# Performance work log

Measured on AMD Instinct MI355X. Metric: run time of the kernel, lower is better.

Reference implementation:

```python
import jax, jax.numpy as jnp
import numpy as np

NEG_SLOPE = 0.2

def gat_conv(x, W, att_src, att_dst, src, dst, num_nodes, concat):
    # x: [N, F_in], W: [F_in, H*C], att_*: [H, C]
    H, C = att_src.shape
    h = (x @ W).reshape(-1, H, C)                      # [N, H, C]
    a_src = jnp.sum(h * att_src[None], axis=-1)        # [N, H]
    a_dst = jnp.sum(h * att_dst[None], axis=-1)        # [N, H]
    # per-edge raw attention: alpha_j (source) + alpha_i (target)
    alpha = a_src[src] + a_dst[dst]                    # [E, H]
    alpha = jax.nn.leaky_relu(alpha, NEG_SLOPE)
    # segment softmax over incoming edges of each destination node
    amax = jax.ops.segment_max(alpha, dst, num_segments=num_nodes)  # [N, H]
    amax = jnp.where(jnp.isfinite(amax), amax, 0.0)
    ex = jnp.exp(alpha - amax[dst])                    # [E, H]
    denom = jax.ops.segment_sum(ex, dst, num_segments=num_nodes)    # [N, H]
    attn = ex / (denom[dst] + 1e-16)                   # [E, H]
    # attention-weighted scatter-add aggregation
    msg = h[src] * attn[..., None]                     # [E, H, C]
    out = jax.ops.segment_sum(msg, dst, num_segments=num_nodes)     # [N, H, C]
    if concat:
        return out.reshape(num_nodes, H * C)
    return out.mean(axis=1)


def setup_inputs() -> dict:
    key = jax.random.key(0)
    ks = jax.random.split(key, 8)
    N, E = 100000, 1600000
    F_in, Hid, Hd, F_out = 256, 32, 8, 64
    glorot = lambda k, shape: jax.random.uniform(
        k, shape, jnp.float32, -1.0, 1.0) * jnp.sqrt(6.0 / (shape[0] + shape[-1]))
    x = jax.random.normal(ks[0], (N, F_in), jnp.float32)
    edge_index = jax.random.randint(ks[1], (2, E), 0, N, jnp.int64)
    W1 = glorot(ks[2], (F_in, Hd * Hid))
    att_src1 = glorot(ks[3], (Hd, Hid))
    att_dst1 = glorot(ks[4], (Hd, Hid))
    W2 = glorot(ks[5], (Hd * Hid, 1 * F_out))
    att_src2 = glorot(ks[6], (1, F_out))
    att_dst2 = glorot(ks[7], (1, F_out))
    return {"x": x, "W1": W1, "att_src1": att_src1, "att_dst1": att_dst1,
            "W2": W2, "att_src2": att_src2, "att_dst2": att_dst2,
            "edge_index": edge_index}


def reference(x, W1, att_src1, att_dst1, W2, att_src2, att_dst2, edge_index):
    src, dst = edge_index[0], edge_index[1]
    N = x.shape[0]
    # dropout is inactive in eval mode
    h = gat_conv(x, W1, att_src1, att_dst1, src, dst, N, concat=True)
    h = jax.nn.elu(h)
    out = gat_conv(h, W2, att_src2, att_dst2, src, dst, N, concat=False)
    return out
```

## Files before the change

kernel.cpp:

```cpp
#include <hip/hip_runtime.h>
#include <hip/hip_bf16.h>

#define LRELU(a) ((a) >= 0.0f ? (a) : 0.2f * (a))

typedef __attribute__((ext_vector_type(8))) _Float16 f16x8;
typedef __attribute__((ext_vector_type(4))) _Float16 f16x4;
typedef __attribute__((ext_vector_type(4))) float f32x4;

__global__ __launch_bounds__(256) void cvt_w_t(const float* __restrict__ W,
                                               _Float16* __restrict__ T,
                                               int K, int Nc) {
    int t = blockIdx.x * 256 + threadIdx.x;
    if (t >= K * Nc) return;
    int k = t / Nc, n = t % Nc;
    T[n * K + k] = (_Float16)W[t];
}

__global__ __launch_bounds__(512) void gemm1_mfma(
    const float* __restrict__ A,
    const _Float16* __restrict__ BT,
    const float* __restrict__ attS, const float* __restrict__ attD,
    _Float16* __restrict__ C, float* __restrict__ a_src, float* __restrict__ a_dst,
    int M) {
    const int K = 256;
    __shared__ _Float16 sA[128][40];
    __shared__ _Float16 sB[256][40];
    int tid = threadIdx.x;
    int m0 = blockIdx.y * 128;
    int wid = tid >> 6, lane = tid & 63;
    int wm = (wid >> 2) * 64, wn = (wid & 3) * 64;
    int lr = lane & 15, lg = lane >> 4;

    f32x4 acc[4][4];
    #pragma unroll
    for (int i = 0; i < 4; ++i)
        #pragma unroll
        for (int j = 0; j < 4; ++j)
            acc[i][j] = (f32x4){0.f, 0.f, 0.f, 0.f};

    for (int k0 = 0; k0 < K; k0 += 32) {
        {
            int row = tid >> 2, seg = tid & 3;
            int grow = m0 + row;
            float4 v0 = make_float4(0.f, 0.f, 0.f, 0.f), v1 = v0;
            if (grow < M) {
                v0 = *(const float4*)&A[(size_t)grow * K + k0 + seg * 8];
                v1 = *(const float4*)&A[(size_t)grow * K + k0 + seg * 8 + 4];
            }
            f16x8 hv;
            hv[0] = (_Float16)v0.x; hv[1] = (_Float16)v0.y;
            hv[2] = (_Float16)v0.z; hv[3] = (_Float16)v0.w;
            hv[4] = (_Float16)v1.x; hv[5] = (_Float16)v1.y;
            hv[6] = (_Float16)v1.z; hv[7] = (_Float16)v1.w;
            *(f16x8*)&sA[row][seg * 8] = hv;
        }
        #pragma unroll
        for (int rnd = 0; rnd < 2; ++rnd) {
            int idx = tid + rnd * 512;
            int row = idx >> 2, seg = idx & 3;
            *(f16x8*)&sB[row][seg * 8] = *(const f16x8*)&BT[(size_t)row * K + k0 + seg * 8];
        }
        __syncthreads();
        f16x8 bfr[4];
        #pragma unroll
        for (int i = 0; i < 4; ++i)
            bfr[i] = *(const f16x8*)&sB[wn + i * 16 + lr][lg * 8];
        #pragma unroll
        for (int mi = 0; mi < 4; ++mi) {
            f16x8 av = *(const f16x8*)&sA[wm + mi * 16 + lr][lg * 8];
            #pragma unroll
            for (int ni = 0; ni < 4; ++ni)
                acc[mi][ni] = __builtin_amdgcn_mfma_f32_16x16x32_f16(av, bfr[ni], acc[mi][ni], 0, 0, 0);
        }
        __syncthreads();
    }

    float asv[4], adv[4];
    #pragma unroll
    for (int ni = 0; ni < 4; ++ni) {
        int col = wn + ni * 16 + lr;
        asv[ni] = attS[col];
        adv[ni] = attD[col];
    }
    int head0 = wn >> 5;
    #pragma unroll
    for (int mi = 0; mi < 4; ++mi) {
        #pragma unroll
        for (int r = 0; r < 4; ++r) {
            int row = m0 + wm + mi * 16 + lg * 4 + r;
            float v0 = acc[mi][0][r], v1 = acc[mi][1][r];
            float v2 = acc[mi][2][r], v3 = acc[mi][3][r];
            float ps0 = v0 * asv[0] + v1 * asv[1], pd0 = v0 * adv[0] + v1 * adv[1];
            float ps1 = v2 * asv[2] + v3 * asv[3], pd1 = v2 * adv[2] + v3 * adv[3];
            #pragma unroll
            for (int msk = 8; msk >= 1; msk >>= 1) {
                ps0 += __shfl_xor(ps0, msk); pd0 += __shfl_xor(pd0, msk);
                ps1 += __shfl_xor(ps1, msk); pd1 += __shfl_xor(pd1, msk);
            }
            if (row < M) {
                C[(size_t)row * 256 + wn +  0 + lr] = (_Float16)v0;
                C[(size_t)row * 256 + wn + 16 + lr] = (_Float16)v1;
                C[(size_t)row * 256 + wn + 32 + lr] = (_Float16)v2;
                C[(size_t)row * 256 + wn + 48 + lr] = (_Float16)v3;
                if (lr == 0) {
                    a_src[(size_t)row * 8 + head0]     = ps0;
                    a_dst[(size_t)row * 8 + head0]     = pd0;
                    a_src[(size_t)row * 8 + head0 + 1] = ps1;
                    a_dst[(size_t)row * 8 + head0 + 1] = pd1;
                }
            }
        }
    }
}

__global__ __launch_bounds__(256) void gemm2_mfma(
    const _Float16* __restrict__ A,
    const _Float16* __restrict__ BT,
    const float* __restrict__ attS, const float* __restrict__ attD,
    _Float16* __restrict__ C, float* __restrict__ a_src, float* __restrict__ a_dst,
    int M) {
    const int K = 256;
    __shared__ _Float16 sA[128][40];
    __shared__ _Float16 sB[64][40];
    int tid = threadIdx.x;
    int m0 = blockIdx.y * 128;
    int wid = tid >> 6, lane = tid & 63;
    int wm = wid * 32;
    int lr = lane & 15, lg = lane >> 4;

    f32x4 acc[2][4];
    #pragma unroll
    for (int i = 0; i < 2; ++i)
        #pragma unroll
        for (int j = 0; j < 4; ++j)
            acc[i][j] = (f32x4){0.f, 0.f, 0.f, 0.f};

    for (int k0 = 0; k0 < K; k0 += 32) {
        #pragma unroll
        for (int rnd = 0; rnd < 2; ++rnd) {
            int idx = tid + rnd * 256;
            int row = idx >> 2, seg = idx & 3;
            int grow = m0 + row;
            f16x8 va = {0, 0, 0, 0, 0, 0, 0, 0};
            if (grow < M) va = *(const f16x8*)&A[(size_t)grow * K + k0 + seg * 8];
            *(f16x8*)&sA[row][seg * 8] = va;
        }
        {
            int row = tid >> 2, seg = tid & 3;
            *(f16x8*)&sB[row][seg * 8] = *(const f16x8*)&BT[(size_t)row * K + k0 + seg * 8];
        }
        __syncthreads();
        f16x8 bfr[4];
        #pragma unroll
        for (int i = 0; i < 4; ++i)
            bfr[i] = *(const f16x8*)&sB[i * 16 + lr][lg * 8];
        #pragma unroll
        for (int mi = 0; mi < 2; ++mi) {
            f16x8 av = *(const f16x8*)&sA[wm + mi * 16 + lr][lg * 8];
            #pragma unroll
            for (int ni = 0; ni < 4; ++ni)
                acc[mi][ni] = __builtin_amdgcn_mfma_f32_16x16x32_f16(av, bfr[ni], acc[mi][ni], 0, 0, 0);
        }
        __syncthreads();
    }

    float asv[4], adv[4];
    #pragma unroll
    for (int ni = 0; ni < 4; ++ni) {
        asv[ni] = attS[ni * 16 + lr];
        adv[ni] = attD[ni * 16 + lr];
    }
    #pragma unroll
    for (int mi = 0; mi < 2; ++mi) {
        #pragma unroll
        for (int r = 0; r < 4; ++r) {
            int row = m0 + wm + mi * 16 + lg * 4 + r;
            float ps = 0.f, pd = 0.f;
            #pragma unroll
            for (int ni = 0; ni < 4; ++ni) {
                float v = acc[mi][ni][r];
                ps += v * asv[ni];
                pd += v * adv[ni];
            }
            #pragma unroll
            for (int msk = 8; msk >= 1; msk >>= 1) {
                ps += __shfl_xor(ps, msk);
                pd += __shfl_xor(pd, msk);
            }
            if (row < M) {
                #pragma unroll
                for (int ni = 0; ni < 4; ++ni)
                    C[(size_t)row * 64 + ni * 16 + lr] = (_Float16)acc[mi][ni][r];
                if (lr == 0) { a_src[row] = ps; a_dst[row] = pd; }
            }
        }
    }
}

__global__ __launch_bounds__(256) void hist_dst(const int* __restrict__ dst, unsigned* __restrict__ cnt, int E) {
    int e = blockIdx.x * 256 + threadIdx.x;
    if (e < E) atomicAdd(&cnt[dst[e]], 1u);
}

__global__ __launch_bounds__(256) void scan_partial(const unsigned* __restrict__ cnt,
                                                    int* __restrict__ rowptr,
                                                    unsigned* __restrict__ bsum, int n) {
    __shared__ unsigned s[256];
    int i = blockIdx.x * 256 + threadIdx.x;
    unsigned v = (i < n) ? cnt[i] : 0u;
    s[threadIdx.x] = v;
    __syncthreads();
    #pragma unroll
    for (int off = 1; off < 256; off <<= 1) {
        unsigned t = (threadIdx.x >= off) ? s[threadIdx.x - off] : 0u;
        __syncthreads();
        s[threadIdx.x] += t;
        __syncthreads();
    }
    if (i < n) rowptr[i + 1] = (int)s[threadIdx.x];
    if (threadIdx.x == 255) bsum[blockIdx.x] = s[255];
}

__global__ __launch_bounds__(512) void scan_bsum(unsigned* __restrict__ bsum, int nb) {
    __shared__ unsigned s[512];
    int t = threadIdx.x;
    s[t] = (t < nb) ? bsum[t] : 0u;
    __syncthreads();
    #pragma unroll
    for (int off = 1; off < 512; off <<= 1) {
        unsigned v = (t >= off) ? s[t - off] : 0u;
        __syncthreads();
        s[t] += v;
        __syncthreads();
    }
    unsigned ex = (t == 0) ? 0u : s[t - 1];
    if (t < nb) bsum[t] = ex;
}

__global__ __launch_bounds__(256) void scan_add(int* __restrict__ rowptr, const unsigned* __restrict__ boff, int n) {
    int i = blockIdx.x * 256 + threadIdx.x;
    if (i < n) rowptr[i + 1] += (int)boff[blockIdx.x];
    if (blockIdx.x == 0 && threadIdx.x == 0) rowptr[0] = 0;
}

__global__ __launch_bounds__(256) void scatter_srcs(const int* __restrict__ src, const int* __restrict__ dst,
                                                    const int* __restrict__ rowptr,
                                                    unsigned* __restrict__ cnt, int* __restrict__ srcs, int E) {
    int e = blockIdx.x * 256 + threadIdx.x;
    if (e >= E) return;
    int d = dst[e];
    unsigned p = atomicAdd(&cnt[d], 1u);
    srcs[rowptr[d] + (int)p] = src[e];
}

__global__ __launch_bounds__(256) void agg1(const int* __restrict__ srcs,
                                            const int* __restrict__ rowptr,
                                            const float* __restrict__ a_src,
                                            const float* __restrict__ a_dst,
                                            const _Float16* __restrict__ h1,
                                            _Float16* __restrict__ o1, int N) {
    int wid = threadIdx.x >> 6;
    int lane = threadIdx.x & 63;
    int d = blockIdx.x * 4 + wid;
    if (d >= N) return;
    int beg = rowptr[d], end = rowptr[d + 1];
    int e8 = lane & 7;
    int hd = lane >> 3;
    float adst = a_dst[(size_t)d * 8 + hd];
    const char* h1b = (const char*)h1;
    const char* asb = (const char*)a_src;
    unsigned loff = (unsigned)(lane << 3);

    float4 acc = make_float4(0.f, 0.f, 0.f, 0.f);
    float wsum = 0.0f;
    for (int j0 = beg; j0 < end; j0 += 8) {
        int nb = end - j0; if (nb > 8) nb = 8;
        int s2 = 0; float w = 0.f;
        if (e8 < nb) {
            s2 = srcs[j0 + e8];
            float a = *(const float*)(asb + (((unsigned)s2 << 5) + ((unsigned)hd << 2))) + adst;
            a = LRELU(a);
            w = __expf(a);
        }
        wsum += w;
        #pragma unroll 8
        for (int t = 0; t < 8; ++t) {
            if (t >= nb) break;
            int sl = (lane & 56) | t;
            float at = __shfl(w, sl);
            int s = __shfl(s2, sl);
            f16x4 hq = *(const f16x4*)(h1b + (((unsigned)s << 9) + loff));
            acc.x += (float)hq[0] * at;
            acc.y += (float)hq[1] * at;
            acc.z += (float)hq[2] * at;
            acc.w += (float)hq[3] * at;
        }
    }
    wsum += __shfl_xor(wsum, 1);
    wsum += __shfl_xor(wsum, 2);
    wsum += __shfl_xor(wsum, 4);
    float rw = 1.0f / (wsum + 1e-16f);
    acc.x *= rw; acc.y *= rw; acc.z *= rw; acc.w *= rw;
    acc.x = acc.x > 0.0f ? acc.x : expm1f(acc.x);
    acc.y = acc.y > 0.0f ? acc.y : expm1f(acc.y);
    acc.z = acc.z > 0.0f ? acc.z : expm1f(acc.z);
    acc.w = acc.w > 0.0f ? acc.w : expm1f(acc.w);
    f16x4 hh;
    hh[0] = (_Float16)acc.x;
    hh[1] = (_Float16)acc.y;
    hh[2] = (_Float16)acc.z;
    hh[3] = (_Float16)acc.w;
    *(f16x4*)(o1 + (size_t)d * 256 + lane * 4) = hh;
}

__global__ __launch_bounds__(256) void agg2(const int* __restrict__ srcs,
                                            const int* __restrict__ rowptr,
                                            const float* __restrict__ a_src,
                                            const float* __restrict__ a_dst,
                                            const _Float16* __restrict__ h2,
                                            float* __restrict__ out, int N) {
    int wid = threadIdx.x >> 6;
    int lane = threadIdx.x & 63;
    int d = blockIdx.x * 4 + wid;
    if (d >= N) return;
    int beg = rowptr[d], end = rowptr[d + 1];
    float adst = a_dst[d];
    const char* h2b = (const char*)h2;
    int grp = lane >> 4;
    int cid = lane & 15;

    float4 acc = make_float4(0.f, 0.f, 0.f, 0.f);
    float wsum = 0.0f;
    for (int j0 = beg; j0 < end; j0 += 64) {
        int nb = end - j0; if (nb > 64) nb = 64;
        int s2 = 0; float w = 0.f;
        if (lane < nb) {
            s2 = srcs[j0 + lane];
            float a = LRELU(a_src[s2] + adst);
            w = __expf(a);
        }
        wsum += w;
        int tmax = (nb + 3) >> 2;
        for (int t = 0; t < tmax; ++t) {
            int ei = 4 * t + grp;
            float at = __shfl(w, ei);
            int s = __shfl(s2, ei);
            f16x4 hv = *(const f16x4*)(h2b + (((unsigned)s << 7) + ((unsigned)cid << 3)));
            acc.x += (float)hv[0] * at;
            acc.y += (float)hv[1] * at;
            acc.z += (float)hv[2] * at;
            acc.w += (float)hv[3] * at;
        }
    }
    #pragma unroll
    for (int mask = 16; mask <= 32; mask <<= 1) {
        acc.x += __shfl_xor(acc.x, mask);
        acc.y += __shfl_xor(acc.y, mask);
        acc.z += __shfl_xor(acc.z, mask);
        acc.w += __shfl_xor(acc.w, mask);
    }
    #pragma unroll
    for (int mask = 1; mask < 64; mask <<= 1)
        wsum += __shfl_xor(wsum, mask);
    float rw = 1.0f / (wsum + 1e-16f);
    if (lane < 16) {
        float4 o = make_float4(acc.x * rw, acc.y * rw, acc.z * rw, acc.w * rw);
        *(float4*)(out + (size_t)d * 64 + cid * 4) = o;
    }
}

extern "C" void kernel_launch(void* const* d_in, const int* in_sizes, int n_in,
                              void* d_out, int out_size, void* d_ws, size_t ws_size,
                              hipStream_t stream) {
    const float* x        = (const float*)d_in[0];
    const float* W1       = (const float*)d_in[1];
    const float* att_src1 = (const float*)d_in[2];
    const float* att_dst1 = (const float*)d_in[3];
    const float* W2       = (const float*)d_in[4];
    const float* att_src2 = (const float*)d_in[5];
    const float* att_dst2 = (const float*)d_in[6];
    const int*   ei       = (const int*)d_in[7];

    int N = in_sizes[0] / 256;
    int E = in_sizes[7] / 2;
    const int* src = ei;
    const int* dst = ei + E;

    _Float16* out1 = (_Float16*)d_ws;
    _Float16* h1f  = out1 + (size_t)N * 256;
    float* a_src1v = (float*)(h1f + (size_t)N * 256);
    float* a_dst1v = a_src1v + (size_t)N * 8;
    float* a_src2v = a_dst1v + (size_t)N * 8;
    float* a_dst2v = a_src2v + N;
    int*   rowptr  = (int*)(a_dst2v + N);
    unsigned* cnt  = (unsigned*)(rowptr + N + 1);
    int*   srcs    = (int*)(cnt + N);
    unsigned* bsum = (unsigned*)(srcs + E);
    _Float16* w1t  = (_Float16*)(bsum + 512);
    _Float16* w2t  = w1t + 65536;

    _Float16* h2f = h1f;

    float* outf = (float*)d_out;
    int nb = (N + 255) / 256;

    hipMemsetAsync(cnt, 0, (size_t)N * sizeof(unsigned), stream);
    hist_dst<<<(E + 255) / 256, 256, 0, stream>>>(dst, cnt, E);
    scan_partial<<<nb, 256, 0, stream>>>(cnt, rowptr, bsum, N);
    scan_bsum<<<1, 512, 0, stream>>>(bsum, nb);
    scan_add<<<nb, 256, 0, stream>>>(rowptr, bsum, N);
    hipMemsetAsync(cnt, 0, (size_t)N * sizeof(unsigned), stream);
    scatter_srcs<<<(E + 255) / 256, 256, 0, stream>>>(src, dst, rowptr, cnt, srcs, E);

    cvt_w_t<<<(65536 + 255) / 256, 256, 0, stream>>>(W1, w1t, 256, 256);
    cvt_w_t<<<(16384 + 255) / 256, 256, 0, stream>>>(W2, w2t, 256, 64);

    gemm1_mfma<<<dim3(1, (N + 127) / 128), 512, 0, stream>>>(x, w1t,
                                                             att_src1, att_dst1,
                                                             h1f, a_src1v, a_dst1v, N);
    agg1<<<(N + 3) / 4, 256, 0, stream>>>(srcs, rowptr, a_src1v, a_dst1v, h1f, out1, N);

    gemm2_mfma<<<dim3(1, (N + 127) / 128), 256, 0, stream>>>(out1, w2t,
                                                             att_src2, att_dst2,
                                                             h2f, a_src2v, a_dst2v, N);
    agg2<<<(N + 3) / 4, 256, 0, stream>>>(srcs, rowptr, a_src2v, a_dst2v, h2f, outf, N);
}
```

Baseline: 486.3 us.

## Reuse histogram atomics for CSR scatter, batch agg1 gathers, merge weight conversion

The histogram kernel now records each edge's atomic slot, so the scatter pass no longer needs a second memset and a second round of atomics. The two weight-conversion launches are merged into one kernel. agg1 gets a full-batch path that issues all eight row gathers before accumulating, which raises memory-level parallelism. The cost is an extra E-sized position buffer that is written and then read back, and the rowptr pointer is split into separate begin/end arguments.

New measurement: 390.7 us, median of 2. 19.6% less time.

```diff
diff --git a/kernel.cpp b/kernel.cpp
--- a/kernel.cpp
+++ b/kernel.cpp
@@ -7,13 +7,21 @@
 typedef __attribute__((ext_vector_type(4))) _Float16 f16x4;
 typedef __attribute__((ext_vector_type(4))) float f32x4;
 
-__global__ __launch_bounds__(256) void cvt_w_t(const float* __restrict__ W,
-                                               _Float16* __restrict__ T,
-                                               int K, int Nc) {
+__global__ __launch_bounds__(256) void cvt_w_both(const float* __restrict__ W1,
+                                                  const float* __restrict__ W2,
+                                                  _Float16* __restrict__ T1,
+                                                  _Float16* __restrict__ T2) {
     int t = blockIdx.x * 256 + threadIdx.x;
-    if (t >= K * Nc) return;
-    int k = t / Nc, n = t % Nc;
-    T[n * K + k] = (_Float16)W[t];
+    if (t < 65536) {
+        int k = t >> 8, n = t & 255;
+        T1[n * 256 + k] = (_Float16)W1[t];
+    } else {
+        int u = t - 65536;
+        if (u < 16384) {
+            int k = u >> 6, n = u & 63;
+            T2[n * 256 + k] = (_Float16)W2[u];
+        }
+    }
 }
 
 __global__ __launch_bounds__(512) void gemm1_mfma(
@@ -197,9 +205,10 @@
     }
 }
 
-__global__ __launch_bounds__(256) void hist_dst(const int* __restrict__ dst, unsigned* __restrict__ cnt, int E) {
+__global__ __launch_bounds__(256) void hist_dst(const int* __restrict__ dst, unsigned* __restrict__ cnt,
+                                                int* __restrict__ pos, int E) {
     int e = blockIdx.x * 256 + threadIdx.x;
-    if (e < E) atomicAdd(&cnt[dst[e]], 1u);
+    if (e < E) pos[e] = (int)atomicAdd(&cnt[dst[e]], 1u);
 }
 
 __global__ __launch_bounds__(256) void scan_partial(const unsigned* __restrict__ cnt,
@@ -244,17 +253,16 @@
 }
 
 __global__ __launch_bounds__(256) void scatter_srcs(const int* __restrict__ src, const int* __restrict__ dst,
-                                                    const int* __restrict__ rowptr,
-                                                    unsigned* __restrict__ cnt, int* __restrict__ srcs, int E) {
+                                                    const int* __restrict__ rowptr, const int* __restrict__ pos,
+                                                    int* __restrict__ srcs, int E) {
     int e = blockIdx.x * 256 + threadIdx.x;
     if (e >= E) return;
-    int d = dst[e];
-    unsigned p = atomicAdd(&cnt[d], 1u);
-    srcs[rowptr[d] + (int)p] = src[e];
+    srcs[rowptr[dst[e]] + pos[e]] = src[e];
 }
 
 __global__ __launch_bounds__(256) void agg1(const int* __restrict__ srcs,
-                                            const int* __restrict__ rowptr,
+                                            const int* __restrict__ begA,
+                                            const int* __restrict__ endB,
                                             const float* __restrict__ a_src,
                                             const float* __restrict__ a_dst,
                                             const _Float16* __restrict__ h1,
@@ -263,7 +271,7 @@
     int lane = threadIdx.x & 63;
     int d = blockIdx.x * 4 + wid;
     if (d >= N) return;
-    int beg = rowptr[d], end = rowptr[d + 1];
+    int beg = begA[d], end = endB[d];
     int e8 = lane & 7;
     int hd = lane >> 3;
     float adst = a_dst[(size_t)d * 8 + hd];
@@ -274,7 +282,7 @@
     float4 acc = make_float4(0.f, 0.f, 0.f, 0.f);
     float wsum = 0.0f;
     for (int j0 = beg; j0 < end; j0 += 8) {
-        int nb = end - j0; if (nb > 8) nb = 8;
+        int nb = end - j0;
         int s2 = 0; float w = 0.f;
         if (e8 < nb) {
             s2 = srcs[j0 + e8];
@@ -283,17 +291,36 @@
             w = __expf(a);
         }
         wsum += w;
-        #pragma unroll 8
-        for (int t = 0; t < 8; ++t) {
-            if (t >= nb) break;
-            int sl = (lane & 56) | t;
-            float at = __shfl(w, sl);
-            int s = __shfl(s2, sl);
-            f16x4 hq = *(const f16x4*)(h1b + (((unsigned)s << 9) + loff));
-            acc.x += (float)hq[0] * at;
-            acc.y += (float)hq[1] * at;
-            acc.z += (float)hq[2] * at;
-            acc.w += (float)hq[3] * at;
+        if (nb >= 8) {
+            float at[8]; unsigned sb[8];
+            #pragma unroll
+            for (int t = 0; t < 8; ++t) {
+                int sl = (lane & 56) | t;
+                at[t] = __shfl(w, sl);
+                sb[t] = ((unsigned)__shfl(s2, sl)) << 9;
+            }
+            f16x4 hv[8];
+            #pragma unroll
+            for (int t = 0; t < 8; ++t)
+                hv[t] = *(const f16x4*)(h1b + (sb[t] + loff));
+            #pragma unroll
+            for (int t = 0; t < 8; ++t) {
+                acc.x += (float)hv[t][0] * at[t];
+                acc.y += (float)hv[t][1] * at[t];
+                acc.z += (float)hv[t][2] * at[t];
+                acc.w += (float)hv[t][3] * at[t];
+            }
+        } else {
+            for (int t = 0; t < nb; ++t) {
+                int sl = (lane & 56) | t;
+                float at = __shfl(w, sl);
+                int s = __shfl(s2, sl);
+                f16x4 hq = *(const f16x4*)(h1b + (((unsigned)s << 9) + loff));
+                acc.x += (float)hq[0] * at;
+                acc.y += (float)hq[1] * at;
+                acc.z += (float)hq[2] * at;
+                acc.w += (float)hq[3] * at;
+            }
         }
     }
     wsum += __shfl_xor(wsum, 1);
@@ -314,7 +341,8 @@
 }
 
 __global__ __launch_bounds__(256) void agg2(const int* __restrict__ srcs,
-                                            const int* __restrict__ rowptr,
+                                            const int* __restrict__ begA,
+                                            const int* __restrict__ endB,
                                             const float* __restrict__ a_src,
                                             const float* __restrict__ a_dst,
                                             const _Float16* __restrict__ h2,
@@ -323,7 +351,7 @@
     int lane = threadIdx.x & 63;
     int d = blockIdx.x * 4 + wid;
     if (d >= N) return;
-    int beg = rowptr[d], end = rowptr[d + 1];
+    int beg = begA[d], end = endB[d];
     float adst = a_dst[d];
     const char* h2b = (const char*)h2;
     int grp = lane >> 4;
@@ -394,9 +422,10 @@
     float* a_dst2v = a_src2v + N;
     int*   rowptr  = (int*)(a_dst2v + N);
     unsigned* cnt  = (unsigned*)(rowptr + N + 1);
-    int*   srcs    = (int*)(cnt + N);
-    unsigned* bsum = (unsigned*)(srcs + E);
-    _Float16* w1t  = (_Float16*)(bsum + 512);
+    unsigned* bsum = cnt + N;
+    int*   pos     = (int*)(bsum + 512);
+    int*   srcs    = pos + E;
+    _Float16* w1t  = (_Float16*)(srcs + E);
     _Float16* w2t  = w1t + 65536;
 
     _Float16* h2f = h1f;
@@ -405,23 +434,21 @@
     int nb = (N + 255) / 256;
 
     hipMemsetAsync(cnt, 0, (size_t)N * sizeof(unsigned), stream);
-    hist_dst<<<(E + 255) / 256, 256, 0, stream>>>(dst, cnt, E);
+    hist_dst<<<(E + 255) / 256, 256, 0, stream>>>(dst, cnt, pos, E);
     scan_partial<<<nb, 256, 0, stream>>>(cnt, rowptr, bsum, N);
     scan_bsum<<<1, 512, 0, stream>>>(bsum, nb);
     scan_add<<<nb, 256, 0, stream>>>(rowptr, bsum, N);
-    hipMemsetAsync(cnt, 0, (size_t)N * sizeof(unsigned), stream);
-    scatter_srcs<<<(E + 255) / 256, 256, 0, stream>>>(src, dst, rowptr, cnt, srcs, E);
-
-    cvt_w_t<<<(65536 + 255) / 256, 256, 0, stream>>>(W1, w1t, 256, 256);
-    cvt_w_t<<<(16384 + 255) / 256, 256, 0, stream>>>(W2, w2t, 256, 64);
+    scatter_srcs<<<(E + 255) / 256, 256, 0, stream>>>(src, dst, rowptr, pos, srcs, E);
+
+    cvt_w_both<<<(65536 + 16384 + 255) / 256, 256, 0, stream>>>(W1, W2, w1t, w2t);
 
     gemm1_mfma<<<dim3(1, (N + 127) / 128), 512, 0, stream>>>(x, w1t,
                                                              att_src1, att_dst1,
                                                              h1f, a_src1v, a_dst1v, N);
-    agg1<<<(N + 3) / 4, 256, 0, stream>>>(srcs, rowptr, a_src1v, a_dst1v, h1f, out1, N);
+    agg1<<<(N + 3) / 4, 256, 0, stream>>>(srcs, rowptr, rowptr + 1, a_src1v, a_dst1v, h1f, out1, N);
 
     gemm2_mfma<<<dim3(1, (N + 127) / 128), 256, 0, stream>>>(out1, w2t,
                                                              att_src2, att_dst2,
                                                              h2f, a_src2v, a_dst2v, N);
-    agg2<<<(N + 3) / 4, 256, 0, stream>>>(srcs, rowptr, a_src2v, a_dst2v, h2f, outf, N);
-}
+    agg2<<<(N + 3) / 4, 256, 0, stream>>>(srcs, rowptr, rowptr + 1, a_src2v, a_dst2v, h2f, outf, N);
+}
```
